# Kernel tuning notes

Measured on AMD Instinct MI355X. Metric: run time of the kernel, lower is better.

## Reference

```python
import jax, jax.numpy as jnp
import numpy as np

EMBED_DIM = 512
NUM_HEADS = 8
EXPAND = 2
D1 = EXPAND * EMBED_DIM          # 1024, already divisible by NUM_HEADS
HEAD_DIM = D1 // NUM_HEADS       # 128
RPE_DIM = 512
RPE_LAYERS = 3
N = 56
M = 56
BATCH = 8
EPS = 1e-8


def simple_rms(x):
    # SimpleRMSNorm: x / (||x||_2 / sqrt(d) + eps), no learned params
    d = x.shape[-1]
    norm = jnp.linalg.norm(x, axis=-1, keepdims=True)
    return x / (norm * (d ** -0.5) + EPS)


def setup_inputs() -> dict:
    key = jax.random.key(0)
    ks = jax.random.split(key, 16)
    def nrm(k, shape, std=0.02):
        return jax.random.normal(k, shape, dtype=jnp.float32) * std
    return {
        'x': jax.random.normal(ks[0], (BATCH, N, M, EMBED_DIM), dtype=jnp.float32),
        'W_u': nrm(ks[1], (D1, EMBED_DIM)),
        'b_u': nrm(ks[2], (D1,)),
        'W_v': nrm(ks[3], (D1, EMBED_DIM)),
        'b_v': nrm(ks[4], (D1,)),
        'W_o': nrm(ks[5], (EMBED_DIM, D1)),
        'b_o': nrm(ks[6], (EMBED_DIM,)),
        'rpe_in_w': nrm(ks[7], (RPE_DIM, 2), 0.5),
        'rpe_in_b': nrm(ks[8], (RPE_DIM,), 0.5),
        'rpe_h_w': nrm(ks[9], (RPE_LAYERS, RPE_DIM, RPE_DIM), 0.05),
        'rpe_h_b': nrm(ks[10], (RPE_LAYERS, RPE_DIM), 0.05),
        'rpe_out_w': nrm(ks[11], (NUM_HEADS * HEAD_DIM, RPE_DIM), 0.05),
        'rpe_out_b': nrm(ks[12], (NUM_HEADS * HEAD_DIM,), 0.05),
        'H': N,
        'W': M,
    }


# static relative-coordinate grid: dp in [-(N-1), N-1], dq in [-(M-1), M-1], par_type=1 (raw indices)
_DP = np.arange(-(N - 1), N, dtype=np.float32)
_DQ = np.arange(-(M - 1), M, dtype=np.float32)
_COORDS = np.stack(np.meshgrid(_DP, _DQ, indexing='ij'), axis=-1)  # (2N-1, 2M-1, 2)
# circulant-embedding placement indices (static)
_RI = ((np.arange(2 * N - 1) - (N - 1)) % (2 * N))
_CI = ((np.arange(2 * M - 1) - (M - 1)) % (2 * M))


def rpe_coeffs(rpe_in_w, rpe_in_b, rpe_h_w, rpe_h_b, rpe_out_w, rpe_out_b):
    # small MLP on relative 2D offsets -> Toeplitz coefficients per head/dim
    t = jnp.asarray(_COORDS) @ rpe_in_w.T + rpe_in_b              # (2N-1, 2M-1, RPE_DIM)
    for i in range(RPE_LAYERS):                                   # residual=False
        t = jax.nn.relu(simple_rms(t)) @ rpe_h_w[i].T + rpe_h_b[i]
    g = jax.nn.relu(simple_rms(t)) @ rpe_out_w.T + rpe_out_b      # (2N-1, 2M-1, h*d)
    g = g.reshape(2 * N - 1, 2 * M - 1, NUM_HEADS, HEAD_DIM)
    return g.transpose(2, 0, 1, 3)                                # (h, 2N-1, 2M-1, d)


def tno2d(v, g):
    # v: (b, h, N, M, d); g: (h, 2N-1, 2M-1, d) Toeplitz coefficients
    # 2D Toeplitz matrix-vector product via circulant embedding + rFFT2
    a = jnp.zeros((NUM_HEADS, 2 * N, 2 * M, HEAD_DIM), dtype=g.dtype)
    a = a.at[:, _RI[:, None], _CI[None, :], :].set(g)
    vf = jnp.fft.rfft2(v, s=(2 * N, 2 * M), axes=(2, 3))          # (b, h, 2N, M+1..., d)
    af = jnp.fft.rfft2(a, axes=(1, 2))                            # (h, 2N, ..., d)
    y = jnp.fft.irfft2(vf * af[None], s=(2 * N, 2 * M), axes=(2, 3))
    return y[:, :, :N, :M, :]


def reference(x, W_u, b_u, W_v, b_v, W_o, b_o,
              rpe_in_w, rpe_in_b, rpe_h_w, rpe_h_b, rpe_out_w, rpe_out_b, H, W):
    # token_shift_type=-1: no shift; H, W unused by the original forward body
    shortcut = x
    xn = simple_rms(x)                                            # pre_norm (SimpleRMSNorm)
    u = jax.nn.silu(xn @ W_u.T + b_u)                             # (b, N, M, D1)
    v = jax.nn.silu(xn @ W_v.T + b_v)                             # (b, N, M, D1)
    b = v.shape[0]
    v = v.reshape(b, N, M, NUM_HEADS, HEAD_DIM).transpose(0, 3, 1, 2, 4)  # b h n m d
    g = rpe_coeffs(rpe_in_w, rpe_in_b, rpe_h_w, rpe_h_b, rpe_out_w, rpe_out_b)
    y = tno2d(v, g)                                               # b h n m d
    y = y.transpose(0, 2, 3, 1, 4).reshape(b, N, M, D1)           # b n m (h d)
    out = u * y
    return out @ W_o.T + b_o + shortcut
```

## Files before the change

### kernel.cpp

```cpp
#include <hip/hip_runtime.h>
#include <math.h>

#define NB 8
#define NN 56
#define POS 3136
#define ROWS 25088
#define GR 111
#define GROWS 12321
#define FREQ 16640

#define OFF_MVT    0u
#define OFF_M2T    28672u
#define OFF_RT2T   57344u
#define OFF_RTC    64960u
#define OFF_MG     79392u
#define OFF_RTCAH  136224u
#define OFF_RTCAL  140384u
#define OFF_MVAH   144544u
#define OFF_MVAL   160928u
#define OFF_M2AH   177312u
#define OFF_M2AL   191648u
#define OFF_RT2BH  205984u
#define OFF_RT2BL  210592u
#define OFF_NINV   215200u
#define OFF_SINV   240288u
#define OFF_WB     252624u
#define OFF_TB16   1694416u
#define OFF_POOL   4848592u
#define WS_FLOATS  9124816u
#define OFF_XN16   9124816u
#define OFF_WUV    15547344u
#define OFF_BUV    16071632u
#define WS_EXT     16073680u
#define OFF_UYF    16073680u
#define WS_EXT2    28918736u
#define GH_STRIDE_US   1818624u
#define TGF_STRIDE_US  1863680u
#define GHAT_STRIDE_US 2129920u
#define OFF_GHA    28918736u
#define OFF_GLA    36193232u
#define OFF_TGFHA  43467728u
#define OFF_TGFLA  50922448u
#define OFF_GHATA  28918736u
#define WS_EXT3    58377168u
#define WB_WU  0u
#define WB_WV  524288u
#define WB_WO  1048576u
#define WB_WH  1572864u
#define WB_WRO 2359296u
#define POOL_U16   1064960u
#define POOL_VCM   2670592u
#define POOL_GH    0u
#define POOL_GL    909312u
#define POOL_TGFH  1818624u
#define POOL_TGFL  2750464u

typedef __attribute__((ext_vector_type(8))) short bf8_t;
typedef __attribute__((ext_vector_type(8))) unsigned short us8_t;
typedef __attribute__((ext_vector_type(4))) float f4_t;

__device__ inline float bf2f(unsigned short b) {
    union { unsigned u; float f; } v; v.u = ((unsigned)b) << 16; return v.f;
}
__device__ inline unsigned short f2bf(float f) {
    union { float f; unsigned u; } v; v.f = f;
    unsigned r = v.u + 0x7FFF + ((v.u >> 16) & 1);
    return (unsigned short)(r >> 16);
}

__global__ void probe_k(float* out, float code) { out[0] = code; }

__global__ void consts_k(float* RTc, float* MvT, float* Mg, float* M2cT, float* RT2cT) {
    int idx = blockIdx.x * 256 + threadIdx.x;
    const float STEP = 0.049087385212340526f;
    if (idx < 14430) {
        int q = idx / 130, col = idx % 130;
        int a = (col < 65) ? col : col - 65;
        float th = (float)((a * q) & 127) * STEP;
        RTc[idx] = (col < 65) ? cosf(th) : -sinf(th);
        return;
    }
    idx -= 14430;
    if (idx < 28672) {
        int s = idx / 256, r = idx % 256;
        int kp = (r < 128) ? r : r - 128;
        int sp = (s < 56) ? s : s - 56;
        float th = (float)((kp * sp) & 127) * STEP;
        float cv = cosf(th), sv = sinf(th);
        MvT[idx] = (r < 128) ? ((s < 56) ? cv : sv) : ((s < 56) ? -sv : cv);
        return;
    }
    idx -= 28672;
    if (idx < 56832) {
        int r = idx / 222, s = idx % 222;
        int kp = (r < 128) ? r : r - 128;
        int sp = (s < 111) ? s : s - 111;
        float th = (float)((kp * sp) & 127) * STEP;
        float cv = cosf(th), sv = sinf(th);
        Mg[idx] = (r < 128) ? ((s < 111) ? cv : sv) : ((s < 111) ? -sv : cv);
        return;
    }
    idx -= 56832;
    if (idx < 28672) {
        int s = idx / 112, r = idx % 112;
        int a = (r < 56) ? (r + 55) : (r - 1);
        int kp = (s < 128) ? s : s - 128;
        float th = (float)((kp * a) & 127) * STEP;
        float cv = cosf(th), sv = sinf(th);
        M2cT[idx] = (r < 56) ? ((s < 128) ? cv : -sv) : ((s < 128) ? sv : cv);
        return;
    }
    idx -= 28672;
    if (idx < 7616) {
        int b = idx / 136, col = idx % 136;
        float val = 0.f;
        if (col < 65 || (col >= 68 && col < 133)) {
            int kq = (col < 65) ? col : col - 68;
            float w = (kq == 0 || kq == 64) ? 1.f : 2.f;
            float th = (float)((kq * (b + 55)) & 127) * STEP;
            val = ((col < 65) ? cosf(th) : -sinf(th)) * w * (1.f / 16384.f);
        }
        RT2cT[idx] = val;
    }
}

__global__ void consts2_k(const float* __restrict__ MvT, const float* __restrict__ M2cT,
                          const float* __restrict__ RT2cT,
                          unsigned short* RTcAh, unsigned short* RTcAl,
                          unsigned short* MvAh, unsigned short* MvAl,
                          unsigned short* M2Ah, unsigned short* M2Al,
                          unsigned short* RT2Bh, unsigned short* RT2Bl) {
    int idx = blockIdx.x * 256 + threadIdx.x;
    const float STEP = 0.049087385212340526f;
    float v = 0.f; unsigned short *ph, *pl; int off;
    if (idx < 8320) {
        int row = idx >> 6, q = idx & 63;
        if (q < 56) {
            int kq = (row < 65) ? row : row - 65;
            float th = (float)((kq * q) & 127) * STEP;
            v = (row < 65) ? cosf(th) : -sinf(th);
        }
        ph = RTcAh; pl = RTcAl; off = idx;
    } else if (idx < 41088) {
        int i = idx - 8320; int r = i >> 7, s = i & 127;
        if (s < 112) v = MvT[s * 256 + r];
        ph = MvAh; pl = MvAl; off = i;
    } else if (idx < 69760) {
        int i = idx - 41088; int a = i >> 8, r = i & 255;
        v = M2cT[r * 112 + a];
        ph = M2Ah; pl = M2Al; off = i;
    } else if (idx < 78976) {
        int i = idx - 69760; int bq = i / 144, col = i % 144;
        if (bq < 56) {
            if (col < 65) v = RT2cT[bq * 136 + col];
            else if (col >= 72 && col < 137) v = RT2cT[bq * 136 + 68 + (col - 72)];
        }
        ph = RT2Bh; pl = RT2Bl; off = i;
    } else return;
    unsigned short h = f2bf(v);
    ph[off] = h;
    pl[off] = f2bf(v - bf2f(h));
}

__global__ void norms_k(const float* __restrict__ X, float* __restrict__ out, int rows) {
    int row = blockIdx.x * 4 + (threadIdx.x >> 6);
    int lane = threadIdx.x & 63;
    if (row >= rows) return;
    const float* p = X + (size_t)row * 512;
    float s = 0.f;
    #pragma unroll
    for (int i = 0; i < 8; ++i) { float v = p[lane + 64 * i]; s += v * v; }
    #pragma unroll
    for (int o = 32; o > 0; o >>= 1) s += __shfl_down(s, o, 64);
    if (lane == 0) out[row] = 1.f / (sqrtf(s) * 0.04419417382415922f + 1e-8f);
}

__global__ void t0_k(const float* __restrict__ w, const float* __restrict__ b, float* __restrict__ out) {
    int idx = blockIdx.x * 256 + threadIdx.x;
    if (idx >= GROWS * 512) return;
    int r = idx >> 9, c = idx & 511;
    int i = r / 111, j = r % 111;
    float dp = (float)(i - 55), dq = (float)(j - 55);
    out[idx] = dp * w[c * 2] + dq * w[c * 2 + 1] + b[c];
}

__global__ void convw_k(const float* __restrict__ src, unsigned short* __restrict__ dst, int n) {
    int i = blockIdx.x * 256 + threadIdx.x;
    if (i < n) dst[i] = f2bf(src[i]);
}
__global__ void convt_k(const float* __restrict__ t, const float* __restrict__ sinv,
                        unsigned short* __restrict__ dst) {
    int i = blockIdx.x * 256 + threadIdx.x;
    if (i >= GROWS * 512) return;
    int r = i >> 9;
    dst[i] = f2bf(fmaxf(t[i], 0.f) * sinv[r]);
}

__global__ void convx_k(const float* __restrict__ x, const float* __restrict__ ninv,
                        unsigned short* __restrict__ xn) {
    int i = blockIdx.x * 256 + threadIdx.x;
    if (i >= ROWS * 64) return;
    int r = i >> 6, c8 = (i & 63) << 3;
    float s = ninv[r];
    const float* p = x + (size_t)r * 512 + c8;
    float4 f1 = *(const float4*)p, f2 = *(const float4*)(p + 4);
    us8_t o;
    o[0] = f2bf(f1.x * s); o[1] = f2bf(f1.y * s);
    o[2] = f2bf(f1.z * s); o[3] = f2bf(f1.w * s);
    o[4] = f2bf(f2.x * s); o[5] = f2bf(f2.y * s);
    o[6] = f2bf(f2.z * s); o[7] = f2bf(f2.w * s);
    *(us8_t*)(xn + (size_t)i * 8) = o;
}

__global__ void convuv_k(const float* __restrict__ Wu, const float* __restrict__ Wv,
                         const float* __restrict__ bu, const float* __restrict__ bv,
                         unsigned short* __restrict__ wuv, float* __restrict__ buv) {
    int i = blockIdx.x * 256 + threadIdx.x;
    if (i < 1048576) {
        int row = i >> 9, k = i & 511;
        int h = row >> 8, j = row & 255;
        float v = (j < 128) ? Wu[(size_t)(h * 128 + j) * 512 + k]
                            : Wv[(size_t)(h * 128 + j - 128) * 512 + k];
        wuv[i] = f2bf(v);
    }
    if (i < 2048) {
        int h = i >> 8, j = i & 255;
        buv[i] = (j < 128) ? bu[h * 128 + j] : bv[h * 128 + j - 128];
    }
}

__global__ __launch_bounds__(256) void mgemm_k(
    const void* __restrict__ Aptr, const unsigned short* __restrict__ B, int ldb,
    const unsigned short* __restrict__ yv, const float* __restrict__ scale,
    int relu_in, int amode,
    void* __restrict__ Cptr, const float* __restrict__ bias,
    const float* __restrict__ xres, float* __restrict__ outAcc, int first,
    int emode, int M, int N, int K)
{
    __shared__ __align__(16) unsigned short As[4096];
    __shared__ __align__(16) unsigned short Bs[4096];
    const int t = threadIdx.x;
    const int lane = t & 63;
    const int quad = lane >> 4, ln = lane & 15;
    const int wave = t >> 6;
    const int wm = (wave >> 1) << 6, wn = (wave & 1) << 6;
    const int row0 = blockIdx.y << 7, col0 = blockIdx.x << 7;
    const int sc = t & 3;
    const int sm = t >> 2;
    const float* Af = (const float*)Aptr;
    const unsigned short* Au = (const unsigned short*)Aptr;
    f4_t acc[4][4];
    #pragma unroll
    for (int i = 0; i < 4; ++i)
        #pragma unroll
        for (int j = 0; j < 4; ++j)
            acc[i][j] = (f4_t){0.f, 0.f, 0.f, 0.f};

    for (int k0 = 0; k0 < K; k0 += 32) {
        #pragma unroll
        for (int rep = 0; rep < 2; ++rep) {
            const int m = sm + (rep << 6);
            const int am = row0 + m;
            us8_t av = {0, 0, 0, 0, 0, 0, 0, 0};
            if (am < M) {
                if (amode == 0) {
                    const float s = scale ? scale[am] : 1.f;
                    const float* ap = Af + (size_t)am * K + k0 + (sc << 3);
                    float4 f1 = *(const float4*)ap;
                    float4 f2 = *(const float4*)(ap + 4);
                    if (relu_in) {
                        f1.x = fmaxf(f1.x, 0.f); f1.y = fmaxf(f1.y, 0.f);
                        f1.z = fmaxf(f1.z, 0.f); f1.w = fmaxf(f1.w, 0.f);
                        f2.x = fmaxf(f2.x, 0.f); f2.y = fmaxf(f2.y, 0.f);
                        f2.z = fmaxf(f2.z, 0.f); f2.w = fmaxf(f2.w, 0.f);
                    }
                    av[0] = f2bf(f1.x * s); av[1] = f2bf(f1.y * s);
                    av[2] = f2bf(f1.z * s); av[3] = f2bf(f1.w * s);
                    av[4] = f2bf(f2.x * s); av[5] = f2bf(f2.y * s);
                    av[6] = f2bf(f2.z * s); av[7] = f2bf(f2.w * s);
                } else if (amode == 1) {
                    av = *(const us8_t*)(Au + (size_t)am * K + k0 + (sc << 3));
                } else {
                    const unsigned short* up = Au + (size_t)am * K + k0 + (sc << 3);
                    const int bb = am / POS, pos = am - bb * POS;
                    const unsigned short* yb = yv + ((size_t)(bb * 128 + k0 + (sc << 3))) * POS + pos;
                    #pragma unroll
                    for (int j = 0; j < 8; ++j)
                        av[j] = f2bf(bf2f(up[j]) * bf2f(yb[(size_t)j * POS]));
                }
            }
            *(us8_t*)&As[(sc << 10) + (m << 3)] = av;
        }
        #pragma unroll
        for (int rep = 0; rep < 2; ++rep) {
            const int n = sm + (rep << 6);
            us8_t bv = *(const us8_t*)(B + (size_t)(col0 + n) * ldb + k0 + (sc << 3));
            *(us8_t*)&Bs[(sc << 10) + (n << 3)] = bv;
        }
        __syncthreads();
        bf8_t af[4], bfr[4];
        #pragma unroll
        for (int i = 0; i < 4; ++i)
            af[i] = *(const bf8_t*)&As[(quad << 10) + ((wm + (i << 4) + ln) << 3)];
        #pragma unroll
        for (int i = 0; i < 4; ++i)
            bfr[i] = *(const bf8_t*)&Bs[(quad << 10) + ((wn + (i << 4) + ln) << 3)];
        #pragma unroll
        for (int i = 0; i < 4; ++i)
            #pragma unroll
            for (int j = 0; j < 4; ++j)
                acc[i][j] = __builtin_amdgcn_mfma_f32_16x16x32_bf16(af[i], bfr[j], acc[i][j], 0, 0, 0);
        __syncthreads();
    }
    #pragma unroll
    for (int i = 0; i < 4; ++i) {
        #pragma unroll
        for (int j = 0; j < 4; ++j) {
            #pragma unroll
            for (int rr = 0; rr < 4; ++rr) {
                const int r = row0 + wm + (i << 4) + (quad << 2) + rr;
                const int c = col0 + wn + (j << 4) + ln;
                if (r >= M) continue;
                float v = acc[i][j][rr];
                if (emode == 0) {
                    v += bias[c];
                    ((float*)Cptr)[(size_t)r * N + c] = v;
                } else if (emode == 2) {
                    v += bias[c]; v = v / (1.f + expf(-v));
                    ((unsigned short*)Cptr)[(size_t)r * N + c] = f2bf(v);
                } else if (emode == 4) {
                    v += bias[c]; v = v / (1.f + expf(-v));
                    const int bb = r / POS, pos = r - bb * POS;
                    ((unsigned short*)Cptr)[((size_t)(bb * 128 + c)) * POS + pos] = f2bf(v);
                } else if (emode == 5) {
                    v += bias[c]; v = v / (1.f + expf(-v));
                    unsigned short bv16 = f2bf(v);
                    if (c < 128) {
                        ((unsigned short*)Cptr)[(size_t)r * 128 + c] = bv16;
                    } else {
                        const int bb = r / POS, pos = r - bb * POS;
                        ((unsigned short*)yv)[((size_t)(bb * 128 + (c - 128))) * POS + pos] = bv16;
                    }
                } else {
                    const size_t oi = (size_t)r * 512 + c;
                    v += first ? (bias[c] + xres[oi]) : outAcc[oi];
                    outAcc[oi] = v;
                }
            }
        }
    }
}

__global__ void gtr_k(const float* __restrict__ src, int ld,
                      unsigned short* __restrict__ Gh, unsigned short* __restrict__ Gl) {
    __shared__ float tile[32][33];
    const int z = blockIdx.z;
    src += (size_t)z * 128;
    Gh += (size_t)z * GH_STRIDE_US;
    Gl += (size_t)z * GH_STRIDE_US;
    int s0 = blockIdx.x * 32, d0 = blockIdx.y * 32;
    int tx = threadIdx.x, ty = threadIdx.y;
    #pragma unroll
    for (int i = 0; i < 32; i += 8) {
        int s = s0 + ty + i;
        if (s < GROWS) tile[ty + i][tx] = src[(size_t)s * ld + d0 + tx];
    }
    __syncthreads();
    int s = s0 + tx;
    if (s < GROWS) {
        int p = s / 111, q = s - p * 111;
        #pragma unroll
        for (int i = 0; i < 32; i += 8) {
            int d = d0 + ty + i;
            float v = tile[tx][ty + i];
            unsigned short h = f2bf(v);
            size_t o = (size_t)(d * 111 + p) * 128 + q;
            Gh[o] = h;
            Gl[o] = f2bf(v - bf2f(h));
        }
    }
}

__global__ void pads_k(unsigned short* __restrict__ Gh, unsigned short* __restrict__ Gl,
                       unsigned short* __restrict__ TgFh, unsigned short* __restrict__ TgFl,
                       int nh) {
    int i = blockIdx.x * 256 + threadIdx.x;
    if (i < nh * 16640) {
        int h = i / 16640, r = i % 16640;
        size_t o = (size_t)h * TGF_STRIDE_US + (size_t)r * 112 + 111;
        TgFh[o] = 0; TgFl[o] = 0;
    }
    if (i < nh * 241536) {
        int h = i / 241536, j = i % 241536;
        int r = j / 17, c = 111 + j % 17;
        size_t o = (size_t)h * GH_STRIDE_US + (size_t)r * 128 + c;
        Gh[o] = 0; Gl[o] = 0;
    }
}

__global__ void fusey_k(unsigned short* __restrict__ u, const unsigned short* __restrict__ y) {
    __shared__ unsigned short yt[32][34];
    const int pos0 = blockIdx.x * 32, k0 = blockIdx.y * 32, bb = blockIdx.z;
    const int tx = threadIdx.x, ty = threadIdx.y;
    #pragma unroll
    for (int i = 0; i < 32; i += 8) {
        int k = k0 + ty + i;
        yt[ty + i][tx] = y[((size_t)(bb * 128 + k)) * POS + pos0 + tx];
    }
    __syncthreads();
    #pragma unroll
    for (int i = 0; i < 32; i += 8) {
        size_t r = (size_t)bb * POS + pos0 + ty + i;
        size_t idx = r * 128 + k0 + tx;
        u[idx] = f2bf(bf2f(u[idx]) * bf2f(yt[tx][ty + i]));
    }
}

__global__ void fusey2_k(const unsigned short* __restrict__ u, const unsigned short* __restrict__ y,
                         unsigned short* __restrict__ uyf, int h) {
    __shared__ unsigned short yt[32][34];
    const int pos0 = blockIdx.x * 32, k0 = blockIdx.y * 32, bb = blockIdx.z;
    const int tx = threadIdx.x, ty = threadIdx.y;
    #pragma unroll
    for (int i = 0; i < 32; i += 8) {
        int k = k0 + ty + i;
        yt[ty + i][tx] = y[((size_t)(bb * 128 + k)) * POS + pos0 + tx];
    }
    __syncthreads();
    #pragma unroll
    for (int i = 0; i < 32; i += 8) {
        size_t r = (size_t)bb * POS + pos0 + ty + i;
        unsigned short uv = u[r * 128 + k0 + tx];
        uyf[r * 1024 + h * 128 + k0 + tx] = f2bf(bf2f(uv) * bf2f(yt[tx][ty + i]));
    }
}

__device__ inline float cval(const float* __restrict__ Csrc, int cmode, int row, int kk) {
    if (cmode == 0)
        return (kk < 111 && row < 130) ? Csrc[kk * 130 + row] : 0.f;
    int s = (kk < 112) ? kk : (111 + (kk - 112));
    bool ok = (kk < 112) ? (kk < 111) : (kk < 223);
    return ok ? Csrc[(size_t)row * 222 + s] : 0.f;
}

__global__ __launch_bounds__(256) void hilo_gemm_k(
    const unsigned short* __restrict__ Dh, const unsigned short* __restrict__ Dl,
    const float* __restrict__ Csrc, int cmode, int constIsA,
    unsigned short* __restrict__ C0, unsigned short* __restrict__ C1,
    int omode, int K, unsigned zD, unsigned zC)
{
    __shared__ __align__(16) unsigned short Ash[4096];
    __shared__ __align__(16) unsigned short Asl[4096];
    __shared__ __align__(16) unsigned short Bsh[4096];
    __shared__ __align__(16) unsigned short Bsl[4096];
    const int t = threadIdx.x;
    const int lane = t & 63;
    const int quad = lane >> 4, ln = lane & 15;
    const int wave = t >> 6;
    const int wm = (wave >> 1) << 6, wn = (wave & 1) << 6;
    const int row0 = blockIdx.y << 7, col0 = blockIdx.x << 7;
    const int sc = t & 3, sm = t >> 2;
    const size_t zoffD = (size_t)blockIdx.z * zD, zoffC = (size_t)blockIdx.z * zC;
    Dh += zoffD; Dl += zoffD;
    C0 += zoffC; if (C1) C1 += zoffC;
    f4_t acc[4][4];
    #pragma unroll
    for (int i = 0; i < 4; ++i)
        #pragma unroll
        for (int j = 0; j < 4; ++j)
            acc[i][j] = (f4_t){0.f, 0.f, 0.f, 0.f};

    for (int k0 = 0; k0 < K; k0 += 32) {
        #pragma unroll
        for (int rep = 0; rep < 2; ++rep) {
            const int m = sm + (rep << 6);
            {
                const int gr = row0 + m;
                us8_t hv, lv;
                if (constIsA) {
                    #pragma unroll
                    for (int j = 0; j < 8; ++j) {
                        int kk = k0 + (sc << 3) + j;
                        float v = cval(Csrc, cmode, gr, kk);
                        unsigned short h = f2bf(v);
                        hv[j] = h; lv[j] = f2bf(v - bf2f(h));
                    }
                } else {
                    hv = *(const us8_t*)(Dh + (size_t)gr * K + k0 + (sc << 3));
                    lv = *(const us8_t*)(Dl + (size_t)gr * K + k0 + (sc << 3));
                }
                *(us8_t*)&Ash[(sc << 10) + (m << 3)] = hv;
                *(us8_t*)&Asl[(sc << 10) + (m << 3)] = lv;
            }
            {
                const int gc = col0 + m;
                us8_t hv, lv;
                if (constIsA) {
                    hv = *(const us8_t*)(Dh + (size_t)gc * K + k0 + (sc << 3));
                    lv = *(const us8_t*)(Dl + (size_t)gc * K + k0 + (sc << 3));
                } else {
                    #pragma unroll
                    for (int j = 0; j < 8; ++j) {
                        int kk = k0 + (sc << 3) + j;
                        float v = cval(Csrc, cmode, gc, kk);
                        unsigned short h = f2bf(v);
                        hv[j] = h; lv[j] = f2bf(v - bf2f(h));
                    }
                }
                *(us8_t*)&Bsh[(sc << 10) + (m << 3)] = hv;
                *(us8_t*)&Bsl[(sc << 10) + (m << 3)] = lv;
            }
        }
        __syncthreads();
        bf8_t ah[4], al[4], bh[4], bl[4];
        #pragma unroll
        for (int i = 0; i < 4; ++i) {
            ah[i] = *(const bf8_t*)&Ash[(quad << 10) + ((wm + (i << 4) + ln) << 3)];
            al[i] = *(const bf8_t*)&Asl[(quad << 10) + ((wm + (i << 4) + ln) << 3)];
            bh[i] = *(const bf8_t*)&Bsh[(quad << 10) + ((wn + (i << 4) + ln) << 3)];
            bl[i] = *(const bf8_t*)&Bsl[(quad << 10) + ((wn + (i << 4) + ln) << 3)];
        }
        #pragma unroll
        for (int i = 0; i < 4; ++i)
            #pragma unroll
            for (int j = 0; j < 4; ++j) {
                acc[i][j] = __builtin_amdgcn_mfma_f32_16x16x32_bf16(ah[i], bh[j], acc[i][j], 0, 0, 0);
                acc[i][j] = __builtin_amdgcn_mfma_f32_16x16x32_bf16(ah[i], bl[j], acc[i][j], 0, 0, 0);
                acc[i][j] = __builtin_amdgcn_mfma_f32_16x16x32_bf16(al[i], bh[j], acc[i][j], 0, 0, 0);
            }
        __syncthreads();
    }
    #pragma unroll
    for (int i = 0; i < 4; ++i) {
        #pragma unroll
        for (int j = 0; j < 4; ++j) {
            #pragma unroll
            for (int rr = 0; rr < 4; ++rr) {
                const int r = row0 + wm + (i << 4) + (quad << 2) + rr;
                const int c = col0 + wn + (j << 4) + ln;
                float v = acc[i][j][rr];
                if (omode == 1) {
                    C0[(size_t)r * 256 + c] = f2bf(v);
                } else {
                    if (r < 130) {
                        int kq = (r < 65) ? r : r - 65;
                        int im = (r < 65) ? 0 : 1;
                        int d = c / 111, p = c - d * 111;
                        size_t o = ((size_t)((d * 65 + kq) * 2 + im)) * 112 + p;
                        unsigned short h = f2bf(v);
                        C0[o] = h;
                        C1[o] = f2bf(v - bf2f(h));
                    }
                }
            }
        }
    }
}

__global__ __launch_bounds__(512) void vfft_k(
    unsigned short* __restrict__ vcm, const unsigned short* __restrict__ Ghat,
    const unsigned short* __restrict__ RTcAh, const unsigned short* __restrict__ RTcAl,
    const unsigned short* __restrict__ MvAh,  const unsigned short* __restrict__ MvAl,
    const unsigned short* __restrict__ M2Ah,  const unsigned short* __restrict__ M2Al,
    const unsigned short* __restrict__ RT2Bh, const unsigned short* __restrict__ RT2Bl,
    const float* __restrict__ MvT, const float* __restrict__ M2cT,
    const float* __restrict__ RT2cT)
{
    __shared__ __align__(16) unsigned short Vs[64 * 72];
    __shared__ __align__(16) unsigned short TqT[32 * 136];
    __shared__ __align__(16) unsigned short VhT[32 * 264];
    __shared__ __align__(16) unsigned short QA[64 * 72];
    __shared__ float tmp[424];
    const int tid = threadIdx.x;
    const int lane = tid & 63, wave = tid >> 6;
    const int quad = lane >> 4, ln = lane & 15;
    const int d = blockIdx.x >> 3, b = blockIdx.x & 7;
    unsigned short* chan = vcm + (size_t)(b * 128 + d) * POS;
    const unsigned short* ghd = Ghat + (size_t)d * FREQ;

    for (int i = tid; i < 64 * 72; i += 512) { Vs[i] = 0; QA[i] = 0; }
    {
        int rr = tid >> 4, cc = 112 + (tid & 15);
        if (tid < 512) TqT[rr * 136 + cc] = 0;
    }
    __syncthreads();
    for (int i = tid; i < POS; i += 512) {
        int p = i / 56, q = i - p * 56;
        Vs[p * 72 + q] = chan[i];
    }
    f4_t acc5[2] = { (f4_t){0,0,0,0}, (f4_t){0,0,0,0} };
    __syncthreads();

    if (tid < 56) {
        const unsigned short* vp = Vs + tid * 72;
        float a = 0.f;
        for (int q = 0; q < 56; q += 2) a += bf2f(vp[q]) - bf2f(vp[q + 1]);
        tmp[tid] = a;
    }
    __syncthreads();
    if (tid < 256) {
        float a = 0.f;
        for (int s = 0; s < 56; ++s) a = fmaf(MvT[s * 256 + tid], tmp[s], a);
        tmp[56 + tid] = a;
    }
    __syncthreads();
    if (tid < 128) {
        float vr = tmp[56 + tid], vi = tmp[184 + tid];
        float gr = bf2f(ghd[64 * 256 + tid]), gm = bf2f(ghd[64 * 256 + 128 + tid]);
        tmp[56 + tid] = vr * gr - vi * gm;
        tmp[184 + tid] = vr * gm + vi * gr;
    }
    __syncthreads();
    if (tid < 112) {
        float a = 0.f;
        for (int r = 0; r < 256; ++r) a = fmaf(M2cT[r * 112 + tid], tmp[56 + r], a);
        tmp[312 + tid] = a;
    }
    __syncthreads();
    #pragma unroll
    for (int ti = 0; ti < 2; ++ti) {
        int t = wave * 2 + ti, mt = t >> 2, nt = t & 3;
        int bq = nt * 16 + ln;
        if (bq < 56) {
            float r1 = RT2cT[bq * 136 + 64], r2 = RT2cT[bq * 136 + 132];
            #pragma unroll
            for (int rr = 0; rr < 4; ++rr) {
                int p = mt * 16 + quad * 4 + rr;
                if (p < 56) acc5[ti][rr] += tmp[312 + p] * r1 + tmp[368 + p] * r2;
            }
        }
    }

    for (int ck = 0; ck < 2; ++ck) {
        const int kq0 = ck * 32;
        __syncthreads();
        #pragma unroll
        for (int ti = 0; ti < 2; ++ti) {
            int t = wave * 2 + ti, mt = t >> 2, nt = t & 3;
            int m = mt * 16 + ln;
            int arow = (m >> 5) * 65 + kq0 + (m & 31);
            int pcol = nt * 16 + ln;
            f4_t a = (f4_t){0, 0, 0, 0};
            #pragma unroll
            for (int ks = 0; ks < 2; ++ks) {
                int k0 = ks * 32 + quad * 8;
                bf8_t Ah = *(const bf8_t*)(RTcAh + arow * 64 + k0);
                bf8_t Al = *(const bf8_t*)(RTcAl + arow * 64 + k0);
                bf8_t Bv = *(const bf8_t*)&Vs[pcol * 72 + k0];
                a = __builtin_amdgcn_mfma_f32_16x16x32_bf16(Ah, Bv, a, 0, 0, 0);
                a = __builtin_amdgcn_mfma_f32_16x16x32_bf16(Al, Bv, a, 0, 0, 0);
            }
            if (pcol < 56) {
                #pragma unroll
                for (int rr = 0; rr < 4; ++rr) {
                    int cp = mt * 16 + quad * 4 + rr;
                    TqT[(cp & 31) * 136 + (cp >> 5) * 56 + pcol] = f2bf(a[rr]);
                }
            }
        }
        __syncthreads();
        #pragma unroll
        for (int ti = 0; ti < 4; ++ti) {
            int t = wave * 4 + ti, mt = t >> 1, nt = t & 1;
            int r = mt * 16 + ln, c = nt * 16 + ln;
            f4_t a = (f4_t){0, 0, 0, 0};
            #pragma unroll
            for (int ks = 0; ks < 4; ++ks) {
                int k0 = ks * 32 + quad * 8;
                bf8_t Ah = *(const bf8_t*)(MvAh + r * 128 + k0);
                bf8_t Al = *(const bf8_t*)(MvAl + r * 128 + k0);
                bf8_t Bv = *(const bf8_t*)&TqT[c * 136 + k0];
                a = __builtin_amdgcn_mfma_f32_16x16x32_bf16(Ah, Bv, a, 0, 0, 0);
                a = __builtin_amdgcn_mfma_f32_16x16x32_bf16(Al, Bv, a, 0, 0, 0);
            }
            int r0 = mt * 16 + quad * 4;
            ushort4 st;
            st.x = f2bf(a[0]); st.y = f2bf(a[1]); st.z = f2bf(a[2]); st.w = f2bf(a[3]);
            *(ushort4*)&VhT[c * 264 + r0] = st;
        }
        __syncthreads();
        #pragma unroll
        for (int i = 0; i < 8; ++i) {
            int o = tid + 512 * i;
            int c = o >> 7, kp = o & 127;
            float vr = bf2f(VhT[c * 264 + kp]), vi = bf2f(VhT[c * 264 + 128 + kp]);
            int gi = (kq0 + c) * 256 + kp;
            float gr = bf2f(ghd[gi]), gm = bf2f(ghd[gi + 128]);
            VhT[c * 264 + kp] = f2bf(vr * gr - vi * gm);
            VhT[c * 264 + 128 + kp] = f2bf(vr * gm + vi * gr);
        }
        __syncthreads();
        #pragma unroll
        for (int ti = 0; ti < 2; ++ti) {
            int t = wave * 2 + ti;
            if (t < 14) {
                int mt = t >> 1, nt = t & 1;
                int aa = mt * 16 + ln, c = nt * 16 + ln;
                f4_t a = (f4_t){0, 0, 0, 0};
                #pragma unroll
                for (int ks = 0; ks < 8; ++ks) {
                    int k0 = ks * 32 + quad * 8;
                    bf8_t Ah = *(const bf8_t*)(M2Ah + aa * 256 + k0);
                    bf8_t Al = *(const bf8_t*)(M2Al + aa * 256 + k0);
                    bf8_t Bv = *(const bf8_t*)&VhT[c * 264 + k0];
                    a = __builtin_amdgcn_mfma_f32_16x16x32_bf16(Ah, Bv, a, 0, 0, 0);
                    a = __builtin_amdgcn_mfma_f32_16x16x32_bf16(Al, Bv, a, 0, 0, 0);
                }
                #pragma unroll
                for (int rr = 0; rr < 4; ++rr) {
                    int av_ = mt * 16 + quad * 4 + rr;
                    int p = (av_ < 56) ? av_ : av_ - 56;
                    int reg = (av_ < 56) ? 0 : 32;
                    QA[p * 72 + reg + c] = f2bf(a[rr]);
                }
            }
        }
        __syncthreads();
        #pragma unroll
        for (int ti = 0; ti < 2; ++ti) {
            int t = wave * 2 + ti, mt = t >> 2, nt = t & 3;
            int p = mt * 16 + ln, bq = nt * 16 + ln;
            #pragma unroll
            for (int ks = 0; ks < 2; ++ks) {
                int k0 = ks * 32 + quad * 8;
                bf8_t Aq = *(const bf8_t*)&QA[p * 72 + k0];
                int col = (ks ? 72 : 0) + kq0 + quad * 8;
                bf8_t Bh = *(const bf8_t*)(RT2Bh + bq * 144 + col);
                bf8_t Bl = *(const bf8_t*)(RT2Bl + bq * 144 + col);
                acc5[ti] = __builtin_amdgcn_mfma_f32_16x16x32_bf16(Aq, Bh, acc5[ti], 0, 0, 0);
                acc5[ti] = __builtin_amdgcn_mfma_f32_16x16x32_bf16(Aq, Bl, acc5[ti], 0, 0, 0);
            }
        }
    }
    #pragma unroll
    for (int ti = 0; ti < 2; ++ti) {
        int t = wave * 2 + ti, mt = t >> 2, nt = t & 3;
        int bq = nt * 16 + ln;
        if (bq < 56) {
            #pragma unroll
            for (int rr = 0; rr < 4; ++rr) {
                int p = mt * 16 + quad * 4 + rr;
                if (p < 56) chan[p * 56 + bq] = f2bf(acc5[ti][rr]);
            }
        }
    }
}

extern "C" void kernel_launch(void* const* d_in, const int* in_sizes, int n_in,
                              void* d_out, int out_size, void* d_ws, size_t ws_size,
                              hipStream_t stream) {
    (void)in_sizes; (void)n_in; (void)out_size;
    const float* x         = (const float*)d_in[0];
    const float* W_u       = (const float*)d_in[1];
    const float* b_u       = (const float*)d_in[2];
    const float* W_v       = (const float*)d_in[3];
    const float* b_v       = (const float*)d_in[4];
    const float* W_o       = (const float*)d_in[5];
    const float* b_o       = (const float*)d_in[6];
    const float* rpe_in_w  = (const float*)d_in[7];
    const float* rpe_in_b  = (const float*)d_in[8];
    const float* rpe_h_w   = (const float*)d_in[9];
    const float* rpe_h_b   = (const float*)d_in[10];
    const float* rpe_out_w = (const float*)d_in[11];
    const float* rpe_out_b = (const float*)d_in[12];
    float* out = (float*)d_out;

    if (ws_size < (size_t)WS_FLOATS * 4) {
        probe_k<<<1, 1, 0, stream>>>(out, 1000.0f + (float)((double)ws_size * 1e-6));
        return;
    }
    const bool ext  = ws_size >= (size_t)WS_EXT * 4;
    const bool ext2 = ws_size >= (size_t)WS_EXT2 * 4;
    const bool ext3 = ws_size >= (size_t)WS_EXT3 * 4;
    float* ws    = (float*)d_ws;
    float* MvT   = ws + OFF_MVT;
    float* M2cT  = ws + OFF_M2T;
    float* RT2cT = ws + OFF_RT2T;
    float* RTc   = ws + OFF_RTC;
    float* Mg    = ws + OFF_MG;
    unsigned short* RTcAh = (unsigned short*)(ws + OFF_RTCAH);
    unsigned short* RTcAl = (unsigned short*)(ws + OFF_RTCAL);
    unsigned short* MvAh  = (unsigned short*)(ws + OFF_MVAH);
    unsigned short* MvAl  = (unsigned short*)(ws + OFF_MVAL);
    unsigned short* M2Ah  = (unsigned short*)(ws + OFF_M2AH);
    unsigned short* M2Al  = (unsigned short*)(ws + OFF_M2AL);
    unsigned short* RT2Bh = (unsigned short*)(ws + OFF_RT2BH);
    unsigned short* RT2Bl = (unsigned short*)(ws + OFF_RT2BL);
    float* ninv  = ws + OFF_NINV;
    float* sinv  = ws + OFF_SINV;
    unsigned short* WB  = (unsigned short*)(ws + OFF_WB);
    unsigned short* wub = WB + WB_WU;
    unsigned short* wvb = WB + WB_WV;
    unsigned short* wob = WB + WB_WO;
    unsigned short* whb = WB + WB_WH;
    unsigned short* wrob= WB + WB_WRO;
    unsigned short* tb16= (unsigned short*)(ws + OFF_TB16);
    float* pool  = ws + OFF_POOL;
    unsigned short* Ghat16 = (unsigned short*)pool;
    unsigned short* u16    = (unsigned short*)(pool + POOL_U16);
    unsigned short* vcm16  = (unsigned short*)(pool + POOL_VCM);
    unsigned short* Gh   = (unsigned short*)(pool + POOL_GH);
    unsigned short* Gl   = (unsigned short*)(pool + POOL_GL);
    unsigned short* TgFh = (unsigned short*)(pool + POOL_TGFH);
    unsigned short* TgFl = (unsigned short*)(pool + POOL_TGFL);
    unsigned short* xn16 = (unsigned short*)(ws + OFF_XN16);
    unsigned short* wuv  = (unsigned short*)(ws + OFF_WUV);
    float* buv   = ws + OFF_BUV;
    unsigned short* uyf  = (unsigned short*)(ws + OFF_UYF);
    unsigned short* GhA   = (unsigned short*)(ws + OFF_GHA);
    unsigned short* GlA   = (unsigned short*)(ws + OFF_GLA);
    unsigned short* TgFhA = (unsigned short*)(ws + OFF_TGFHA);
    unsigned short* TgFlA = (unsigned short*)(ws + OFF_TGFLA);
    unsigned short* GhatA = (unsigned short*)(ws + OFF_GHATA);
    float* tA    = out;
    float* tBf   = out + 6308352u;
    float* g_row_all = out;

    consts_k<<<533, 256, 0, stream>>>(RTc, MvT, Mg, M2cT, RT2cT);
    consts2_k<<<309, 256, 0, stream>>>(MvT, M2cT, RT2cT, RTcAh, RTcAl,
                                       MvAh, MvAl, M2Ah, M2Al, RT2Bh, RT2Bl);

    if (ext) {
        convuv_k<<<4096, 256, 0, stream>>>(W_u, W_v, b_u, b_v, wuv, buv);
    } else {
        convw_k<<<2048, 256, 0, stream>>>(W_u, wub, 524288);
        convw_k<<<2048, 256, 0, stream>>>(W_v, wvb, 524288);
    }
    convw_k<<<2048, 256, 0, stream>>>(W_o, wob, 524288);
    convw_k<<<3072, 256, 0, stream>>>(rpe_h_w, whb, 786432);
    convw_k<<<2048, 256, 0, stream>>>(rpe_out_w, wrob, 524288);

    t0_k<<<24642, 256, 0, stream>>>(rpe_in_w, rpe_in_b, tA);
    norms_k<<<3081, 256, 0, stream>>>(tA, sinv, GROWS);
    mgemm_k<<<dim3(4, 97), 256, 0, stream>>>(tA, whb, 512, nullptr, sinv, 1, 0,
        tBf, rpe_h_b, nullptr, nullptr, 0, 0, GROWS, 512, 512);
    norms_k<<<3081, 256, 0, stream>>>(tBf, sinv, GROWS);
    mgemm_k<<<dim3(4, 97), 256, 0, stream>>>(tBf, whb + 262144, 512, nullptr, sinv, 1, 0,
        tA, rpe_h_b + 512, nullptr, nullptr, 0, 0, GROWS, 512, 512);
    norms_k<<<3081, 256, 0, stream>>>(tA, sinv, GROWS);
    mgemm_k<<<dim3(4, 97), 256, 0, stream>>>(tA, whb + 524288, 512, nullptr, sinv, 1, 0,
        tBf, rpe_h_b + 1024, nullptr, nullptr, 0, 0, GROWS, 512, 512);
    norms_k<<<3081, 256, 0, stream>>>(tBf, sinv, GROWS);
    convt_k<<<24642, 256, 0, stream>>>(tBf, sinv, tb16);

    norms_k<<<6272, 256, 0, stream>>>(x, ninv, ROWS);
    if (ext) convx_k<<<6272, 256, 0, stream>>>(x, ninv, xn16);

    mgemm_k<<<dim3(8, 97), 256, 0, stream>>>(tb16, wrob, 512, nullptr, nullptr, 0, 1,
        g_row_all, rpe_out_b, nullptr, nullptr, 0, 0, GROWS, 1024, 512);

    if (ext3) {
        gtr_k<<<dim3(386, 4, 8), dim3(32, 8), 0, stream>>>(g_row_all, 1024, GhA, GlA);
        pads_k<<<7548, 256, 0, stream>>>(GhA, GlA, TgFhA, TgFlA, 8);
        hilo_gemm_k<<<dim3(111, 2, 8), 256, 0, stream>>>(GhA, GlA, RTc, 0, 1,
            TgFhA, TgFlA, 0, 128, GH_STRIDE_US, TGF_STRIDE_US);
        hilo_gemm_k<<<dim3(2, 65, 8), 256, 0, stream>>>(TgFhA, TgFlA, Mg, 1, 0,
            GhatA, nullptr, 1, 224, TGF_STRIDE_US, GHAT_STRIDE_US);
    }

    for (int h = 0; h < 8; ++h) {
        const size_t wo = (size_t)h * 65536;
        const unsigned short* ghat_h = ext3 ? (GhatA + (size_t)h * GHAT_STRIDE_US) : Ghat16;
        if (!ext3) {
            gtr_k<<<dim3(386, 4), dim3(32, 8), 0, stream>>>(g_row_all + h * 128, 1024, Gh, Gl);
            pads_k<<<944, 256, 0, stream>>>(Gh, Gl, TgFh, TgFl, 1);
            hilo_gemm_k<<<dim3(111, 2), 256, 0, stream>>>(Gh, Gl, RTc, 0, 1,
                TgFh, TgFl, 0, 128, 0, 0);
            hilo_gemm_k<<<dim3(2, 65), 256, 0, stream>>>(TgFh, TgFl, Mg, 1, 0,
                Ghat16, nullptr, 1, 224, 0, 0);
        }
        if (ext) {
            mgemm_k<<<dim3(2, 196), 256, 0, stream>>>(xn16, wuv + (size_t)h * 131072, 512,
                vcm16, nullptr, 0, 1,
                u16, buv + h * 256, nullptr, nullptr, 0, 5, ROWS, 256, 512);
        } else {
            mgemm_k<<<dim3(1, 196), 256, 0, stream>>>(x, wvb + wo, 512, nullptr, ninv, 0, 0,
                vcm16, b_v + h * 128, nullptr, nullptr, 0, 4, ROWS, 128, 512);
        }
        vfft_k<<<1024, 512, 0, stream>>>(vcm16, ghat_h, RTcAh, RTcAl, MvAh, MvAl,
            M2Ah, M2Al, RT2Bh, RT2Bl, MvT, M2cT, RT2cT);
        if (!ext) {
            mgemm_k<<<dim3(1, 196), 256, 0, stream>>>(x, wub + wo, 512, nullptr, ninv, 0, 0,
                u16, b_u + h * 128, nullptr, nullptr, 0, 2, ROWS, 128, 512);
        }
        if (ext2) {
            fusey2_k<<<dim3(98, 4, 8), dim3(32, 8), 0, stream>>>(u16, vcm16, uyf, h);
        } else {
            fusey_k<<<dim3(98, 4, 8), dim3(32, 8), 0, stream>>>(u16, vcm16);
            mgemm_k<<<dim3(4, 196), 256, 0, stream>>>(u16, wob + h * 128, 1024, nullptr, nullptr, 0, 1,
                nullptr, b_o, x, out, (h == 0) ? 1 : 0, 3, ROWS, 512, 128);
        }
    }
    if (ext2) {
        mgemm_k<<<dim3(4, 196), 256, 0, stream>>>(uyf, wob, 1024, nullptr, nullptr, 0, 1,
            nullptr, b_o, x, out, 1, 3, ROWS, 512, 1024);
    }
}
```

Before: 2.384 ms.

## Batch all heads into single u/v GEMM, FFT conv and gating launches

```diff
diff --git a/kernel.cpp b/kernel.cpp
--- a/kernel.cpp
+++ b/kernel.cpp
@@ -43,6 +43,9 @@
 #define OFF_TGFLA  50922448u
 #define OFF_GHATA  28918736u
 #define WS_EXT3    58377168u
+#define VCMA_HS    3211264u
+#define OFF_VCMA   58377168u
+#define WS_EXT4    71222224u
 #define WB_WU  0u
 #define WB_WV  524288u
 #define WB_WO  1048576u
@@ -341,6 +344,16 @@
                         const int bb = r / POS, pos = r - bb * POS;
                         ((unsigned short*)yv)[((size_t)(bb * 128 + (c - 128))) * POS + pos] = bv16;
                     }
+                } else if (emode == 6) {
+                    v += bias[c]; v = v / (1.f + expf(-v));
+                    unsigned short bv16 = f2bf(v);
+                    const int hh = c >> 8, j2 = c & 255;
+                    if (j2 < 128) {
+                        ((unsigned short*)Cptr)[(size_t)r * 1024 + hh * 128 + j2] = bv16;
+                    } else {
+                        const int bb = r / POS, pos = r - bb * POS;
+                        ((unsigned short*)yv)[((size_t)(hh * 1024 + bb * 128 + (j2 - 128))) * POS + pos] = bv16;
+                    }
                 } else {
                     const size_t oi = (size_t)r * 512 + c;
                     v += first ? (bias[c] + xres[oi]) : outAcc[oi];
@@ -432,6 +445,27 @@
         size_t r = (size_t)bb * POS + pos0 + ty + i;
         unsigned short uv = u[r * 128 + k0 + tx];
         uyf[r * 1024 + h * 128 + k0 + tx] = f2bf(bf2f(uv) * bf2f(yt[tx][ty + i]));
+    }
+}
+
+__global__ void fusey3_k(unsigned short* __restrict__ uyf, const unsigned short* __restrict__ vcmA) {
+    __shared__ unsigned short yt[32][34];
+    const int pos0 = blockIdx.x * 32, k0 = blockIdx.y * 32;
+    const int z = blockIdx.z;
+    const int h = z >> 3, bb = z & 7;
+    const unsigned short* y = vcmA + (size_t)h * VCMA_HS;
+    const int tx = threadIdx.x, ty = threadIdx.y;
+    #pragma unroll
+    for (int i = 0; i < 32; i += 8) {
+        int k = k0 + ty + i;
+        yt[ty + i][tx] = y[((size_t)(bb * 128 + k)) * POS + pos0 + tx];
+    }
+    __syncthreads();
+    #pragma unroll
+    for (int i = 0; i < 32; i += 8) {
+        size_t r = (size_t)bb * POS + pos0 + ty + i;
+        size_t idx = r * 1024 + h * 128 + k0 + tx;
+        uyf[idx] = f2bf(bf2f(uyf[idx]) * bf2f(yt[tx][ty + i]));
     }
 }
 
@@ -564,7 +598,7 @@
     const unsigned short* __restrict__ M2Ah,  const unsigned short* __restrict__ M2Al,
     const unsigned short* __restrict__ RT2Bh, const unsigned short* __restrict__ RT2Bl,
     const float* __restrict__ MvT, const float* __restrict__ M2cT,
-    const float* __restrict__ RT2cT)
+    const float* __restrict__ RT2cT, unsigned vcmHS, unsigned ghatHS)
 {
     __shared__ __align__(16) unsigned short Vs[64 * 72];
     __shared__ __align__(16) unsigned short TqT[32 * 136];
@@ -574,9 +608,11 @@
     const int tid = threadIdx.x;
     const int lane = tid & 63, wave = tid >> 6;
     const int quad = lane >> 4, ln = lane & 15;
-    const int d = blockIdx.x >> 3, b = blockIdx.x & 7;
-    unsigned short* chan = vcm + (size_t)(b * 128 + d) * POS;
-    const unsigned short* ghd = Ghat + (size_t)d * FREQ;
+    const int zz = blockIdx.x >> 10;
+    const int bid = blockIdx.x & 1023;
+    const int d = bid >> 3, b = bid & 7;
+    unsigned short* chan = vcm + (size_t)zz * vcmHS + (size_t)(b * 128 + d) * POS;
+    const unsigned short* ghd = Ghat + (size_t)zz * ghatHS + (size_t)d * FREQ;
 
     for (int i = tid; i < 64 * 72; i += 512) { Vs[i] = 0; QA[i] = 0; }
     {
@@ -772,6 +808,7 @@
     const bool ext  = ws_size >= (size_t)WS_EXT * 4;
     const bool ext2 = ws_size >= (size_t)WS_EXT2 * 4;
     const bool ext3 = ws_size >= (size_t)WS_EXT3 * 4;
+    const bool ext4 = ws_size >= (size_t)WS_EXT4 * 4;
     float* ws    = (float*)d_ws;
     float* MvT   = ws + OFF_MVT;
     float* M2cT  = ws + OFF_M2T;
@@ -812,6 +849,7 @@
     unsigned short* TgFhA = (unsigned short*)(ws + OFF_TGFHA);
     unsigned short* TgFlA = (unsigned short*)(ws + OFF_TGFLA);
     unsigned short* GhatA = (unsigned short*)(ws + OFF_GHATA);
+    unsigned short* vcmA  = (unsigned short*)(ws + OFF_VCMA);
     float* tA    = out;
     float* tBf   = out + 6308352u;
     float* g_row_all = out;
@@ -858,37 +896,45 @@
             GhatA, nullptr, 1, 224, TGF_STRIDE_US, GHAT_STRIDE_US);
     }
 
-    for (int h = 0; h < 8; ++h) {
-        const size_t wo = (size_t)h * 65536;
-        const unsigned short* ghat_h = ext3 ? (GhatA + (size_t)h * GHAT_STRIDE_US) : Ghat16;
-        if (!ext3) {
-            gtr_k<<<dim3(386, 4), dim3(32, 8), 0, stream>>>(g_row_all + h * 128, 1024, Gh, Gl);
-            pads_k<<<944, 256, 0, stream>>>(Gh, Gl, TgFh, TgFl, 1);
-            hilo_gemm_k<<<dim3(111, 2), 256, 0, stream>>>(Gh, Gl, RTc, 0, 1,
-                TgFh, TgFl, 0, 128, 0, 0);
-            hilo_gemm_k<<<dim3(2, 65), 256, 0, stream>>>(TgFh, TgFl, Mg, 1, 0,
-                Ghat16, nullptr, 1, 224, 0, 0);
-        }
-        if (ext) {
-            mgemm_k<<<dim3(2, 196), 256, 0, stream>>>(xn16, wuv + (size_t)h * 131072, 512,
-                vcm16, nullptr, 0, 1,
-                u16, buv + h * 256, nullptr, nullptr, 0, 5, ROWS, 256, 512);
-        } else {
-            mgemm_k<<<dim3(1, 196), 256, 0, stream>>>(x, wvb + wo, 512, nullptr, ninv, 0, 0,
-                vcm16, b_v + h * 128, nullptr, nullptr, 0, 4, ROWS, 128, 512);
-        }
-        vfft_k<<<1024, 512, 0, stream>>>(vcm16, ghat_h, RTcAh, RTcAl, MvAh, MvAl,
-            M2Ah, M2Al, RT2Bh, RT2Bl, MvT, M2cT, RT2cT);
-        if (!ext) {
-            mgemm_k<<<dim3(1, 196), 256, 0, stream>>>(x, wub + wo, 512, nullptr, ninv, 0, 0,
-                u16, b_u + h * 128, nullptr, nullptr, 0, 2, ROWS, 128, 512);
-        }
-        if (ext2) {
-            fusey2_k<<<dim3(98, 4, 8), dim3(32, 8), 0, stream>>>(u16, vcm16, uyf, h);
-        } else {
-            fusey_k<<<dim3(98, 4, 8), dim3(32, 8), 0, stream>>>(u16, vcm16);
-            mgemm_k<<<dim3(4, 196), 256, 0, stream>>>(u16, wob + h * 128, 1024, nullptr, nullptr, 0, 1,
-                nullptr, b_o, x, out, (h == 0) ? 1 : 0, 3, ROWS, 512, 128);
+    if (ext4) {
+        mgemm_k<<<dim3(16, 196), 256, 0, stream>>>(xn16, wuv, 512, vcmA, nullptr, 0, 1,
+            uyf, buv, nullptr, nullptr, 0, 6, ROWS, 2048, 512);
+        vfft_k<<<8192, 512, 0, stream>>>(vcmA, GhatA, RTcAh, RTcAl, MvAh, MvAl,
+            M2Ah, M2Al, RT2Bh, RT2Bl, MvT, M2cT, RT2cT, VCMA_HS, GHAT_STRIDE_US);
+        fusey3_k<<<dim3(98, 4, 64), dim3(32, 8), 0, stream>>>(uyf, vcmA);
+    } else {
+        for (int h = 0; h < 8; ++h) {
+            const size_t wo = (size_t)h * 65536;
+            const unsigned short* ghat_h = ext3 ? (GhatA + (size_t)h * GHAT_STRIDE_US) : Ghat16;
+            if (!ext3) {
+                gtr_k<<<dim3(386, 4), dim3(32, 8), 0, stream>>>(g_row_all + h * 128, 1024, Gh, Gl);
+                pads_k<<<944, 256, 0, stream>>>(Gh, Gl, TgFh, TgFl, 1);
+                hilo_gemm_k<<<dim3(111, 2), 256, 0, stream>>>(Gh, Gl, RTc, 0, 1,
+                    TgFh, TgFl, 0, 128, 0, 0);
+                hilo_gemm_k<<<dim3(2, 65), 256, 0, stream>>>(TgFh, TgFl, Mg, 1, 0,
+                    Ghat16, nullptr, 1, 224, 0, 0);
+            }
+            if (ext) {
+                mgemm_k<<<dim3(2, 196), 256, 0, stream>>>(xn16, wuv + (size_t)h * 131072, 512,
+                    vcm16, nullptr, 0, 1,
+                    u16, buv + h * 256, nullptr, nullptr, 0, 5, ROWS, 256, 512);
+            } else {
+                mgemm_k<<<dim3(1, 196), 256, 0, stream>>>(x, wvb + wo, 512, nullptr, ninv, 0, 0,
+                    vcm16, b_v + h * 128, nullptr, nullptr, 0, 4, ROWS, 128, 512);
+            }
+            vfft_k<<<1024, 512, 0, stream>>>(vcm16, ghat_h, RTcAh, RTcAl, MvAh, MvAl,
+                M2Ah, M2Al, RT2Bh, RT2Bl, MvT, M2cT, RT2cT, 0, 0);
+            if (!ext) {
+                mgemm_k<<<dim3(1, 196), 256, 0, stream>>>(x, wub + wo, 512, nullptr, ninv, 0, 0,
+                    u16, b_u + h * 128, nullptr, nullptr, 0, 2, ROWS, 128, 512);
+            }
+            if (ext2) {
+                fusey2_k<<<dim3(98, 4, 8), dim3(32, 8), 0, stream>>>(u16, vcm16, uyf, h);
+            } else {
+                fusey_k<<<dim3(98, 4, 8), dim3(32, 8), 0, stream>>>(u16, vcm16);
+                mgemm_k<<<dim3(4, 196), 256, 0, stream>>>(u16, wob + h * 128, 1024, nullptr, nullptr, 0, 1,
+                    nullptr, b_o, x, out, (h == 0) ? 1 : 0, 3, ROWS, 512, 128);
+            }
         }
     }
     if (ext2) {
```

After: 3.642 ms. 52.8% more time.
